# Optimization experiments

Hardware: AMD Instinct MI355X
Metric: run time of the kernel (lower is better)

The kernel has to match this reference:

```python
import jax, jax.numpy as jnp
import numpy as np

B, FNP, D = 16, 4096, 512
P, S, F = 16, 8, 32

def setup_inputs() -> dict:
    key = jax.random.key(0)
    k1, k2 = jax.random.split(key)
    token_states = jax.random.normal(k1, (B, FNP, D), dtype=jnp.float32)
    W = jax.random.normal(k2, (2 * P, D), dtype=jnp.float32) * 0.02
    b = jnp.zeros((2 * P,), dtype=jnp.float32)
    return {"token_states": token_states, "W": W, "b": b, "T": 1032}

def reference(token_states, W, b, T):
    Bsz, FNp, Dm = token_states.shape
    Np = FNp // F
    h = token_states.reshape(Bsz, F, Np, Dm)
    # per-patch linear head: [B, F, Np, 2P]
    raw = jnp.einsum('bfnd,ed->bfne', h, W) + b
    raw = raw.reshape(Bsz, F, Np, 2, P)
    mu = raw[:, :, :, 0, :]                                   # [B, F, Np, P]
    sigma = jnp.clip(jnp.exp(raw[:, :, :, 1, :]), 1e-06, None)
    mu = jnp.transpose(mu, (0, 2, 3, 1))                      # [B, Np, P, F]
    sigma = jnp.transpose(sigma, (0, 2, 3, 1))
    # overlap-add fold: time index for each (patch, offset)
    t = (jnp.arange(Np)[:, None] * S + jnp.arange(P)[None, :]).reshape(-1)  # [Np*P]
    valid = (t < T)
    t_c = jnp.where(valid, t, 0)
    vmask = valid.astype(mu.dtype)[None, :, None]             # [1, Np*P, 1]
    mu_flat = mu.reshape(Bsz, Np * P, F) * vmask
    sg_flat = sigma.reshape(Bsz, Np * P, F) * vmask
    mu_full = jnp.zeros((Bsz, T, F), dtype=mu.dtype).at[:, t_c, :].add(mu_flat)
    sigma_full = jnp.zeros((Bsz, T, F), dtype=mu.dtype).at[:, t_c, :].add(sg_flat)
    counts = jnp.zeros((T,), dtype=mu.dtype).at[t_c].add(valid.astype(mu.dtype))
    counts = jnp.clip(counts, 1.0, None)[None, :, None]       # [1, T, 1]
    return (mu_full / counts, sigma_full / counts)
```

## Files before the change

kernel.cpp:

```cpp
#include <hip/hip_runtime.h>
#include <math.h>

#define B_    16
#define F_    32
#define NP_   128
#define D_    512
#define P_    16
#define KC    32
#define NCH   16
#define BUFW  (NP_ * KC)
#define NRING 8
#define EOFF  (NRING * BUFW)

typedef __attribute__((ext_vector_type(8)))  short  short8;
typedef __attribute__((ext_vector_type(16))) float  floatx16;

union Frag { short8 v; unsigned int u[4]; };

__device__ inline unsigned int cvt_pk_bf16(float lo, float hi) {
    unsigned int r;
    asm volatile("v_cvt_pk_bf16_f32 %0, %1, %2" : "=v"(r) : "v"(lo), "v"(hi));
    return r;
}

#define EBAR asm volatile("s_waitcnt lgkmcnt(0)\n\ts_barrier" ::: "memory")

__global__ __launch_bounds__(512, 4)
void pd_kernel(const float* __restrict__ ts,
               const float* __restrict__ W,
               const float* __restrict__ bias,
               float* __restrict__ out, int T)
{
    __shared__ float smem[EOFF + NP_ * 33];

    const int tid  = threadIdx.x;
    const int lane = tid & 63;
    const int wave = tid >> 6;
    const int mt   = wave & 3;
    const int p    = wave >> 2;

    const int d  = blockIdx.x;
    const int b  = (d & 7) | (((d >> 7) & 1) << 3);
    const int fp = (d >> 3) & 15;
    const float* __restrict__ tsb0 = ts + ((size_t)(b * F_ + 2 * fp) * NP_) * D_;
    const float* __restrict__ tsb1 = tsb0 + (size_t)NP_ * D_;

    auto STAGE = [&](const float* base, int cc) {
#pragma unroll
        for (int it = 0; it < 2; ++it) {
            const int slot = it * 512 + tid;
            const int r2 = slot >> 3;
            const int qg = (slot & 7) ^ (r2 & 7);
            const float* src = base + r2 * D_ + cc * KC + (qg << 2);
            float* dst = smem + (cc & 7) * BUFW + (slot << 2);
            __builtin_amdgcn_global_load_lds(
                (const __attribute__((address_space(1))) unsigned int*)src,
                (__attribute__((address_space(3))) unsigned int*)dst,
                16, 0, 0);
        }
    };

    const int e_b = lane & 31;
    const int kh  = lane >> 5;
    Frag bf[NCH];
    {
        const float* wb = W + (size_t)e_b * D_ + kh * 8;
#pragma unroll
        for (int c = 0; c < NCH; ++c) {
            const int k = c * 32 + p * 16;
            const float4 lo = *(const float4*)(wb + k);
            const float4 hi = *(const float4*)(wb + k + 4);
            bf[c].u[0] = cvt_pk_bf16(lo.x, lo.y);
            bf[c].u[1] = cvt_pk_bf16(lo.z, lo.w);
            bf[c].u[2] = cvt_pk_bf16(hi.x, hi.y);
            bf[c].u[3] = cvt_pk_bf16(hi.z, hi.w);
        }
    }
    __builtin_amdgcn_sched_barrier(0);

#pragma unroll
    for (int c = 0; c < 7; ++c) STAGE(tsb0, c);
    __builtin_amdgcn_sched_barrier(0);

    const int ldsrow = mt * 32 + (lane & 31);
    const int sw8    = ldsrow & 7;
    const int aq     = p * 4 + kh * 2;

    const int TF = T * F_;
    const size_t halfoff = (size_t)B_ * TF;
    float* const E = smem + EOFF;

#pragma unroll
    for (int q = 0; q < 2; ++q) {
        const float* __restrict__ tscur = q ? tsb1 : tsb0;

        floatx16 acc;
#pragma unroll
        for (int r = 0; r < 16; ++r) acc[r] = 0.f;

#pragma unroll
        for (int c = 0; c < NCH; ++c) {
            if (q == 0 || c <= 9)
                asm volatile("s_waitcnt vmcnt(12)\n\ts_barrier" ::: "memory");
            else if (c == 10)
                asm volatile("s_waitcnt vmcnt(10)\n\ts_barrier" ::: "memory");
            else if (c == 11)
                asm volatile("s_waitcnt vmcnt(8)\n\ts_barrier" ::: "memory");
            else if (c == 12)
                asm volatile("s_waitcnt vmcnt(6)\n\ts_barrier" ::: "memory");
            else if (c == 13)
                asm volatile("s_waitcnt vmcnt(4)\n\ts_barrier" ::: "memory");
            else if (c == 14)
                asm volatile("s_waitcnt vmcnt(2)\n\ts_barrier" ::: "memory");
            else
                asm volatile("s_waitcnt vmcnt(0)\n\ts_barrier" ::: "memory");
            __builtin_amdgcn_sched_barrier(0);

            if (q == 0) {
                if (c <= 8) STAGE(tsb0, c + 7);
                else        STAGE(tsb1, c - 9);
            } else {
                if (c <= 8) STAGE(tsb1, c + 7);
            }
            __builtin_amdgcn_sched_barrier(0);

            const float* rowp = smem + (c & 7) * BUFW + ldsrow * KC;
            const float4 lo = *(const float4*)(rowp + ((aq ^ sw8) << 2));
            const float4 hi = *(const float4*)(rowp + (((aq + 1) ^ sw8) << 2));
            Frag a;
            a.u[0] = cvt_pk_bf16(lo.x, lo.y);
            a.u[1] = cvt_pk_bf16(lo.z, lo.w);
            a.u[2] = cvt_pk_bf16(hi.x, hi.y);
            a.u[3] = cvt_pk_bf16(hi.z, hi.w);
            acc = __builtin_amdgcn_mfma_f32_32x32x16_bf16(a.v, bf[c].v, acc, 0, 0, 0);
        }

        const int f = 2 * fp + q;
        if (p == 0) {
#pragma unroll
            for (int r = 0; r < 16; ++r) {
                const int rowl = (r & 3) + 8 * (r >> 2) + 4 * kh;
                E[(mt * 32 + rowl) * 33 + e_b] = acc[r];
            }
        }
        EBAR;
        if (p == 1) {
#pragma unroll
            for (int r = 0; r < 16; ++r) {
                const int rowl = (r & 3) + 8 * (r >> 2) + 4 * kh;
                E[(mt * 32 + rowl) * 33 + e_b] += acc[r];
            }
        }
        EBAR;

#pragma unroll
        for (int jj = 0; jj < 8; ++jj) {
            const int item = tid * 8 + jj;
            const int n = item >> 5;
            const int e = item & 31;
            float v = E[n * 33 + e] + bias[e];
            if (e >= P_) v = fmaxf(expf(v), 1e-6f);
            E[n * 33 + e] = v;
        }
        EBAR;

        for (int item = tid; item < 2 * T; item += 512) {
            const int half = (item >= T) ? 1 : 0;
            const int t    = item - half * T;
            const int nmax = min(NP_ - 1, t >> 3);
            const int nmin = (t > 8) ? ((t - 8) >> 3) : 0;
            float sum = 0.f;
            const int cnt = nmax - nmin + 1;
            for (int nn = nmin; nn <= nmax; ++nn)
                sum += E[nn * 33 + (half << 4) + (t - (nn << 3))];
            const float r = (cnt > 0) ? sum / (float)cnt : 0.f;
            out[(size_t)half * halfoff + (size_t)b * TF + (size_t)t * F_ + f] = r;
        }
    }
}

extern "C" void kernel_launch(void* const* d_in, const int* in_sizes, int n_in,
                              void* d_out, int out_size, void* d_ws, size_t ws_size,
                              hipStream_t stream)
{
    const float* ts   = (const float*)d_in[0];
    const float* W    = (const float*)d_in[1];
    const float* bias = (const float*)d_in[2];
    float* out = (float*)d_out;

    const int T = out_size / (2 * B_ * F_);

    dim3 grid(B_ * F_ / 2);
    dim3 block(512);
    pd_kernel<<<grid, block, 0, stream>>>(ts, W, bias, out, T);
}
```

Baseline: 39.54 us.

## Overlap first frame's epilogue with second frame's GEMM chunks

The first frame's reduction, bias/exp and overlap-add fold now run interleaved across the first seven chunk iterations of the second frame's MFMA loop, using two separate accumulators, rather than serially between frames. The first two loads are issued before the W fragment conversion, and launch bounds drop from 4 to 2 blocks per CU. This hides epilogue latency behind the second frame's loads and MFMAs, at the cost of more live registers and possibly lower occupancy.

Result: faster. 37.16 us (-6.0%).

```diff
diff --git a/kernel.cpp b/kernel.cpp
--- a/kernel.cpp
+++ b/kernel.cpp
@@ -25,7 +25,7 @@
 
 #define EBAR asm volatile("s_waitcnt lgkmcnt(0)\n\ts_barrier" ::: "memory")
 
-__global__ __launch_bounds__(512, 4)
+__global__ __launch_bounds__(512, 2)
 void pd_kernel(const float* __restrict__ ts,
                const float* __restrict__ W,
                const float* __restrict__ bias,
@@ -60,6 +60,10 @@
         }
     };
 
+    STAGE(tsb0, 0);
+    STAGE(tsb0, 1);
+    __builtin_amdgcn_sched_barrier(0);
+
     const int e_b = lane & 31;
     const int kh  = lane >> 5;
     Frag bf[NCH];
@@ -79,7 +83,7 @@
     __builtin_amdgcn_sched_barrier(0);
 
 #pragma unroll
-    for (int c = 0; c < 7; ++c) STAGE(tsb0, c);
+    for (int c = 2; c < 7; ++c) STAGE(tsb0, c);
     __builtin_amdgcn_sched_barrier(0);
 
     const int ldsrow = mt * 32 + (lane & 31);
@@ -90,92 +94,139 @@
     const size_t halfoff = (size_t)B_ * TF;
     float* const E = smem + EOFF;
 
-#pragma unroll
-    for (int q = 0; q < 2; ++q) {
-        const float* __restrict__ tscur = q ? tsb1 : tsb0;
-
-        floatx16 acc;
-#pragma unroll
-        for (int r = 0; r < 16; ++r) acc[r] = 0.f;
-
-#pragma unroll
-        for (int c = 0; c < NCH; ++c) {
-            if (q == 0 || c <= 9)
-                asm volatile("s_waitcnt vmcnt(12)\n\ts_barrier" ::: "memory");
-            else if (c == 10)
-                asm volatile("s_waitcnt vmcnt(10)\n\ts_barrier" ::: "memory");
-            else if (c == 11)
-                asm volatile("s_waitcnt vmcnt(8)\n\ts_barrier" ::: "memory");
-            else if (c == 12)
-                asm volatile("s_waitcnt vmcnt(6)\n\ts_barrier" ::: "memory");
-            else if (c == 13)
-                asm volatile("s_waitcnt vmcnt(4)\n\ts_barrier" ::: "memory");
-            else if (c == 14)
-                asm volatile("s_waitcnt vmcnt(2)\n\ts_barrier" ::: "memory");
-            else
-                asm volatile("s_waitcnt vmcnt(0)\n\ts_barrier" ::: "memory");
-            __builtin_amdgcn_sched_barrier(0);
-
-            if (q == 0) {
-                if (c <= 8) STAGE(tsb0, c + 7);
-                else        STAGE(tsb1, c - 9);
-            } else {
-                if (c <= 8) STAGE(tsb1, c + 7);
-            }
-            __builtin_amdgcn_sched_barrier(0);
-
-            const float* rowp = smem + (c & 7) * BUFW + ldsrow * KC;
-            const float4 lo = *(const float4*)(rowp + ((aq ^ sw8) << 2));
-            const float4 hi = *(const float4*)(rowp + (((aq + 1) ^ sw8) << 2));
-            Frag a;
-            a.u[0] = cvt_pk_bf16(lo.x, lo.y);
-            a.u[1] = cvt_pk_bf16(lo.z, lo.w);
-            a.u[2] = cvt_pk_bf16(hi.x, hi.y);
-            a.u[3] = cvt_pk_bf16(hi.z, hi.w);
-            acc = __builtin_amdgcn_mfma_f32_32x32x16_bf16(a.v, bf[c].v, acc, 0, 0, 0);
-        }
-
-        const int f = 2 * fp + q;
-        if (p == 0) {
-#pragma unroll
-            for (int r = 0; r < 16; ++r) {
-                const int rowl = (r & 3) + 8 * (r >> 2) + 4 * kh;
-                E[(mt * 32 + rowl) * 33 + e_b] = acc[r];
-            }
-        }
-        EBAR;
-        if (p == 1) {
-#pragma unroll
-            for (int r = 0; r < 16; ++r) {
-                const int rowl = (r & 3) + 8 * (r >> 2) + 4 * kh;
-                E[(mt * 32 + rowl) * 33 + e_b] += acc[r];
-            }
-        }
-        EBAR;
-
-#pragma unroll
-        for (int jj = 0; jj < 8; ++jj) {
-            const int item = tid * 8 + jj;
-            const int n = item >> 5;
-            const int e = item & 31;
-            float v = E[n * 33 + e] + bias[e];
-            if (e >= P_) v = fmaxf(expf(v), 1e-6f);
-            E[n * 33 + e] = v;
-        }
-        EBAR;
-
-        for (int item = tid; item < 2 * T; item += 512) {
-            const int half = (item >= T) ? 1 : 0;
-            const int t    = item - half * T;
-            const int nmax = min(NP_ - 1, t >> 3);
-            const int nmin = (t > 8) ? ((t - 8) >> 3) : 0;
-            float sum = 0.f;
-            const int cnt = nmax - nmin + 1;
-            for (int nn = nmin; nn <= nmax; ++nn)
-                sum += E[nn * 33 + (half << 4) + (t - (nn << 3))];
-            const float r = (cnt > 0) ? sum / (float)cnt : 0.f;
-            out[(size_t)half * halfoff + (size_t)b * TF + (size_t)t * F_ + f] = r;
-        }
+    auto COMPUTE = [&](int c, floatx16& acc) {
+        const float* rowp = smem + (c & 7) * BUFW + ldsrow * KC;
+        const float4 lo = *(const float4*)(rowp + ((aq ^ sw8) << 2));
+        const float4 hi = *(const float4*)(rowp + (((aq + 1) ^ sw8) << 2));
+        Frag a;
+        a.u[0] = cvt_pk_bf16(lo.x, lo.y);
+        a.u[1] = cvt_pk_bf16(lo.z, lo.w);
+        a.u[2] = cvt_pk_bf16(hi.x, hi.y);
+        a.u[3] = cvt_pk_bf16(hi.z, hi.w);
+        acc = __builtin_amdgcn_mfma_f32_32x32x16_bf16(a.v, bf[c].v, acc, 0, 0, 0);
+    };
+
+    floatx16 accA, accB;
+#pragma unroll
+    for (int r = 0; r < 16; ++r) { accA[r] = 0.f; accB[r] = 0.f; }
+
+#pragma unroll
+    for (int c = 0; c < NCH; ++c) {
+        asm volatile("s_waitcnt vmcnt(12)\n\ts_barrier" ::: "memory");
+        __builtin_amdgcn_sched_barrier(0);
+        if (c <= 8) STAGE(tsb0, c + 7);
+        else        STAGE(tsb1, c - 9);
+        __builtin_amdgcn_sched_barrier(0);
+        COMPUTE(c, accA);
+    }
+
+    const int f0 = 2 * fp;
+    const int QT = (2 * T + 3) / 4;
+#pragma unroll
+    for (int c = 0; c < NCH; ++c) {
+        if (c <= 9)
+            asm volatile("s_waitcnt vmcnt(12) lgkmcnt(0)\n\ts_barrier" ::: "memory");
+        else if (c == 10)
+            asm volatile("s_waitcnt vmcnt(10)\n\ts_barrier" ::: "memory");
+        else if (c == 11)
+            asm volatile("s_waitcnt vmcnt(8)\n\ts_barrier" ::: "memory");
+        else if (c == 12)
+            asm volatile("s_waitcnt vmcnt(6)\n\ts_barrier" ::: "memory");
+        else if (c == 13)
+            asm volatile("s_waitcnt vmcnt(4)\n\ts_barrier" ::: "memory");
+        else if (c == 14)
+            asm volatile("s_waitcnt vmcnt(2)\n\ts_barrier" ::: "memory");
+        else
+            asm volatile("s_waitcnt vmcnt(0)\n\ts_barrier" ::: "memory");
+        __builtin_amdgcn_sched_barrier(0);
+
+        if (c <= 8) STAGE(tsb1, c + 7);
+        __builtin_amdgcn_sched_barrier(0);
+
+        if (c == 0) {
+            if (p == 0) {
+#pragma unroll
+                for (int r = 0; r < 16; ++r) {
+                    const int rowl = (r & 3) + 8 * (r >> 2) + 4 * kh;
+                    E[(mt * 32 + rowl) * 33 + e_b] = accA[r];
+                }
+            }
+        } else if (c == 1) {
+            if (p == 1) {
+#pragma unroll
+                for (int r = 0; r < 16; ++r) {
+                    const int rowl = (r & 3) + 8 * (r >> 2) + 4 * kh;
+                    E[(mt * 32 + rowl) * 33 + e_b] += accA[r];
+                }
+            }
+        } else if (c == 2) {
+#pragma unroll
+            for (int jj = 0; jj < 8; ++jj) {
+                const int item = tid * 8 + jj;
+                const int n = item >> 5;
+                const int e = item & 31;
+                float v = E[n * 33 + e] + bias[e];
+                if (e >= P_) v = fmaxf(expf(v), 1e-6f);
+                E[n * 33 + e] = v;
+            }
+        } else if (c >= 3 && c <= 6) {
+            const int g  = c - 3;
+            const int hi = min((g + 1) * QT, 2 * T);
+            for (int item = g * QT + tid; item < hi; item += 512) {
+                const int half = (item >= T) ? 1 : 0;
+                const int t    = item - half * T;
+                const int nmax = min(NP_ - 1, t >> 3);
+                const int nmin = (t > 8) ? ((t - 8) >> 3) : 0;
+                float sum = 0.f;
+                const int cnt = nmax - nmin + 1;
+                for (int nn = nmin; nn <= nmax; ++nn)
+                    sum += E[nn * 33 + (half << 4) + (t - (nn << 3))];
+                const float r = (cnt > 0) ? sum / (float)cnt : 0.f;
+                out[(size_t)half * halfoff + (size_t)b * TF + (size_t)t * F_ + f0] = r;
+            }
+        }
+
+        COMPUTE(c, accB);
+    }
+
+    const int f1 = 2 * fp + 1;
+    if (p == 0) {
+#pragma unroll
+        for (int r = 0; r < 16; ++r) {
+            const int rowl = (r & 3) + 8 * (r >> 2) + 4 * kh;
+            E[(mt * 32 + rowl) * 33 + e_b] = accB[r];
+        }
+    }
+    EBAR;
+    if (p == 1) {
+#pragma unroll
+        for (int r = 0; r < 16; ++r) {
+            const int rowl = (r & 3) + 8 * (r >> 2) + 4 * kh;
+            E[(mt * 32 + rowl) * 33 + e_b] += accB[r];
+        }
+    }
+    EBAR;
+#pragma unroll
+    for (int jj = 0; jj < 8; ++jj) {
+        const int item = tid * 8 + jj;
+        const int n = item >> 5;
+        const int e = item & 31;
+        float v = E[n * 33 + e] + bias[e];
+        if (e >= P_) v = fmaxf(expf(v), 1e-6f);
+        E[n * 33 + e] = v;
+    }
+    EBAR;
+    for (int item = tid; item < 2 * T; item += 512) {
+        const int half = (item >= T) ? 1 : 0;
+        const int t    = item - half * T;
+        const int nmax = min(NP_ - 1, t >> 3);
+        const int nmin = (t > 8) ? ((t - 8) >> 3) : 0;
+        float sum = 0.f;
+        const int cnt = nmax - nmin + 1;
+        for (int nn = nmin; nn <= nmax; ++nn)
+            sum += E[nn * 33 + (half << 4) + (t - (nn << 3))];
+        const float r = (cnt > 0) ? sum / (float)cnt : 0.f;
+        out[(size_t)half * halfoff + (size_t)b * TF + (size_t)t * F_ + f1] = r;
     }
 }
 
```
